# Kernel tuning notes

Hardware: AMD Instinct MI355X
Metric: run time of the kernel (lower is better)

Reference implementation:

```python
import jax, jax.numpy as jnp
import numpy as np

B, L, D = 16, 2048, 256
N_POS = (L - 24) // 16            # 126 chunk boundary positions
MAX_SEGS = L // 2 + N_POS + 2     # static upper bound on segments per utterance (=1152)


def setup_inputs() -> dict:
    key = jax.random.key(0)
    k1, k2 = jax.random.split(key, 2)
    xs_pad = jax.random.normal(k1, (B, L, D), jnp.float32)
    olens = jnp.full((B,), L, dtype=jnp.int32)
    w_lin = jax.random.normal(k2, (D, 1), jnp.float32) * 0.05
    b_lin = jnp.zeros((1,), jnp.float32)
    gamma = jnp.ones((D,), jnp.float32)
    beta = jnp.zeros((D,), jnp.float32)
    return {"xs_pad": xs_pad, "olens": olens, "w_lin": w_lin,
            "b_lin": b_lin, "gamma": gamma, "beta": beta}


def _uma_forward(xs_pad, w_lin, b_lin, gamma, beta):
    b, length, d = xs_pad.shape
    positions = 24 + 16 * jnp.arange((length - 24) // 16)  # forced chunk boundaries
    max_segs = length // 2 + positions.shape[0] + 2

    uma = jax.nn.sigmoid(xs_pad @ w_lin + b_lin)           # [B,L,1] attention weights
    w = uma[..., 0]                                        # [B,L]
    wd = jax.lax.stop_gradient(w)                          # mask construction is detached

    # strict local minima (valleys); boundary pads behave as zeros like F.pad in torch
    prev = jnp.pad(wd[:, :-1], ((0, 0), (1, 0)))
    nxt = jnp.pad(wd[:, 1:], ((0, 0), (0, 1)))
    mask = (wd < prev) & (wd < nxt)
    mask = mask.at[:, positions].set(True)                 # chunk-wise boundaries
    mask = mask.at[:, 0].set(True)

    # chunk_counts: number of segment starts within each [start_idx, end_idx) chunk
    t = jnp.arange(length)
    seg_id = jnp.searchsorted(positions, t, side='right')  # which chunk each frame is in
    chunk_counts = jax.vmap(
        lambda m: jax.ops.segment_sum(m.astype(jnp.int32), seg_id,
                                      num_segments=positions.shape[0] + 1))(mask)

    counts = mask.sum(axis=1)                              # segments per batch item (= olens out)

    # segment start indices: sorted positions of True, padded with L for empty slots
    starts = jnp.sort(jnp.where(mask, t, length), axis=1)[:, :max_segs]   # [B,M]
    # segment end indices: start-mask minus index 0, plus index L-1, then +2 clamped to L
    emask = mask.at[:, 0].set(False).at[:, -1].set(True)
    ends = jnp.minimum(jnp.sort(jnp.where(emask, t, length), axis=1)[:, :max_segs] + 2, length)
    ends = jnp.where(starts == length, length, ends)       # padded slots -> empty segment

    # segment sums over [start, end) via exclusive prefix sums (same math as tril-mask bmm)
    alpha_h = uma * xs_pad                                 # [B,L,D]
    pc_x = jnp.pad(jnp.cumsum(alpha_h, axis=1), ((0, 0), (1, 0), (0, 0)))  # [B,L+1,D]
    pc_w = jnp.pad(jnp.cumsum(w, axis=1), ((0, 0), (1, 0)))                # [B,L+1]
    bidx = jnp.arange(b)[:, None]
    num = pc_x[bidx, ends] - pc_x[bidx, starts]            # [B,M,D]
    den = pc_w[bidx, ends] - pc_w[bidx, starts]            # [B,M]
    out = num / jnp.maximum(den, 1e-6)[..., None]

    # LayerNorm (torch default eps=1e-5)
    mu = out.mean(-1, keepdims=True)
    var = ((out - mu) ** 2).mean(-1, keepdims=True)
    out = (out - mu) / jnp.sqrt(var + 1e-5) * gamma + beta
    return out, counts, chunk_counts


def reference(xs_pad, olens, w_lin, b_lin, gamma, beta):
    return _uma_forward(xs_pad, w_lin, b_lin, gamma, beta)
```

## Files before the change

kernel.cpp:

```cpp
#include <hip/hip_runtime.h>
#include <math.h>

#define BB 16
#define LL 2048
#define DD 256
#define NPOS 126
#define NSEG 127
#define MS 1152
#define POS_MAX (24 + 16 * (NPOS - 1))


__global__ __launch_bounds__(256) void k_proj(const float* __restrict__ xs,
                                              const float* __restrict__ w_lin,
                                              const float* __restrict__ b_lin,
                                              float* __restrict__ w) {
    int gtid = blockIdx.x * 256 + threadIdx.x;
    int row  = gtid >> 6;
    int lane = threadIdx.x & 63;
    const float4 x4 = *(const float4*)(xs + (size_t)row * DD + lane * 4);
    const float4 wl = *(const float4*)(w_lin + lane * 4);
    float p = x4.x * wl.x + x4.y * wl.y + x4.z * wl.z + x4.w * wl.w;
    #pragma unroll
    for (int off = 32; off > 0; off >>= 1) p += __shfl_down(p, off, 64);
    if (lane == 0) {
        float x = p + b_lin[0];
        float s = (x >= 0.f) ? 1.f / (1.f + expf(-x))
                             : expf(x) / (1.f + expf(x));
        w[row] = s;
    }
}

__global__ __launch_bounds__(256) void k_mask(const float* __restrict__ w,
                                              int* __restrict__ starts,
                                              int* __restrict__ counts_i,
                                              float* __restrict__ out_counts,
                                              float* __restrict__ out_cc) {
    int b   = blockIdx.x;
    int tid = threadIdx.x;
    __shared__ float sw[LL];
    __shared__ int   scc[NSEG];
    __shared__ int   wave_tot[4];

    for (int i = tid; i < LL; i += 256) sw[i] = w[b * LL + i];
    for (int i = tid; i < NSEG; i += 256) scc[i] = 0;
    __syncthreads();

    int base_t = tid * 8;
    bool bits[8];
    int c = 0;
    #pragma unroll
    for (int j = 0; j < 8; ++j) {
        int t = base_t + j;
        float wd = sw[t];
        float pv = (t > 0)      ? sw[t - 1] : 0.f;
        float nx = (t < LL - 1) ? sw[t + 1] : 0.f;
        bool m = (wd < pv) && (wd < nx);
        if (t == 0) m = true;
        if (t >= 24 && t <= POS_MAX && ((t - 24) & 15) == 0) m = true;
        bits[j] = m;
        c += m ? 1 : 0;
    }

    int lane = tid & 63, wv = tid >> 6;
    int inc = c;
    #pragma unroll
    for (int off = 1; off < 64; off <<= 1) {
        int v = __shfl_up(inc, off, 64);
        if (lane >= off) inc += v;
    }
    if (lane == 63) wave_tot[wv] = inc;
    __syncthreads();
    int wbase = 0;
    for (int i = 0; i < wv; ++i) wbase += wave_tot[i];
    int total = wave_tot[0] + wave_tot[1] + wave_tot[2] + wave_tot[3];
    int rank  = wbase + inc - c;

    #pragma unroll
    for (int j = 0; j < 8; ++j) {
        if (bits[j]) {
            int t = base_t + j;
            starts[b * MS + rank] = t;
            ++rank;
            int sid = (t < 24) ? 0 : min((t - 24) / 16 + 1, NSEG - 1);
            atomicAdd(&scc[sid], 1);
        }
    }
    if (tid == 0) { counts_i[b] = total; out_counts[b] = (float)total; }
    __syncthreads();
    for (int i = total + tid; i < MS; i += 256) starts[b * MS + i] = LL;
    for (int i = tid; i < NSEG; i += 256) out_cc[b * NSEG + i] = (float)scc[i];
}

__global__ __launch_bounds__(256) void k_segs(const float* __restrict__ xs,
                                              const float* __restrict__ w,
                                              const int* __restrict__ starts,
                                              const int* __restrict__ counts_i,
                                              const float* __restrict__ gamma,
                                              const float* __restrict__ beta,
                                              float* __restrict__ out) {
    int gtid = blockIdx.x * 256 + threadIdx.x;
    int seg  = gtid >> 6;
    int lane = threadIdx.x & 63;
    int b = seg / MS, k = seg - b * MS;
    int cnt = counts_i[b];
    float* orow = out + (size_t)seg * DD + lane * 4;
    if (k >= cnt) {
        *(float4*)orow = make_float4(0.f, 0.f, 0.f, 0.f);
        return;
    }
    int start = starts[b * MS + k];
    int end   = (k + 1 < cnt) ? min(starts[b * MS + k + 1] + 2, LL) : LL;

    float4 acc = make_float4(0.f, 0.f, 0.f, 0.f);
    float den = 0.f;
    const float* xrow = xs + ((size_t)(b * LL + start)) * DD + lane * 4;
    for (int t = start; t < end; ++t, xrow += DD) {
        float wt = w[b * LL + t];
        float4 x4 = *(const float4*)xrow;
        acc.x += wt * x4.x; acc.y += wt * x4.y;
        acc.z += wt * x4.z; acc.w += wt * x4.w;
        den += wt;
    }
    float inv = 1.f / fmaxf(den, 1e-6f);
    float4 v = make_float4(acc.x * inv, acc.y * inv, acc.z * inv, acc.w * inv);

    float s = v.x + v.y + v.z + v.w;
    #pragma unroll
    for (int off = 32; off > 0; off >>= 1) s += __shfl_down(s, off, 64);
    s = __shfl(s, 0, 64);
    float mu = s * (1.f / DD);
    float dx = v.x - mu, dy = v.y - mu, dz = v.z - mu, dw = v.w - mu;
    float q = dx * dx + dy * dy + dz * dz + dw * dw;
    #pragma unroll
    for (int off = 32; off > 0; off >>= 1) q += __shfl_down(q, off, 64);
    q = __shfl(q, 0, 64);
    float rstd = rsqrtf(q * (1.f / DD) + 1e-5f);

    float4 g  = *(const float4*)(gamma + lane * 4);
    float4 bt = *(const float4*)(beta + lane * 4);
    float4 o;
    o.x = dx * rstd * g.x + bt.x;
    o.y = dy * rstd * g.y + bt.y;
    o.z = dz * rstd * g.z + bt.z;
    o.w = dw * rstd * g.w + bt.w;
    *(float4*)orow = o;
}

extern "C" void kernel_launch(void* const* d_in, const int* in_sizes, int n_in,
                              void* d_out, int out_size, void* d_ws, size_t ws_size,
                              hipStream_t stream) {
    const float* xs    = (const float*)d_in[0];
    const float* w_lin = (const float*)d_in[2];
    const float* b_lin = (const float*)d_in[3];
    const float* gamma = (const float*)d_in[4];
    const float* beta  = (const float*)d_in[5];

    float* out       = (float*)d_out;
    float* out_cnt   = out + (size_t)BB * MS * DD;
    float* out_cc    = out_cnt + BB;

    float* w         = (float*)d_ws;
    int*   starts    = (int*)((char*)d_ws + (size_t)BB * LL * 4);
    int*   counts_i  = (int*)((char*)d_ws + (size_t)BB * LL * 4 + (size_t)BB * MS * 4);

    k_proj<<<(BB * LL) / 4, 256, 0, stream>>>(xs, w_lin, b_lin, w);
    k_mask<<<BB, 256, 0, stream>>>(w, starts, counts_i, out_cnt, out_cc);
    k_segs<<<(BB * MS) / 4, 256, 0, stream>>>(xs, w, starts, counts_i,
                                              gamma, beta, out);
}
```

Measured before the change: 101.2 us.

## Fuse mask/start computation into segment pooling kernel with redundant per-block scan

Merges the per-batch mask/prefix-scan kernel and the segment pooling+LayerNorm kernel into one launch. Each of 72 blocks per batch item recomputes the valley mask and start indices into shared memory, then handles 16 segment slots, reading weights from shared memory. This drops one launch, the serialized 16-block mask kernel and the global round trip for starts/counts. In exchange the scan is done redundantly per block and there are fewer, longer-running blocks.

```diff
diff --git a/kernel.cpp b/kernel.cpp
--- a/kernel.cpp
+++ b/kernel.cpp
@@ -8,6 +8,8 @@
 #define NSEG 127
 #define MS 1152
 #define POS_MAX (24 + 16 * (NPOS - 1))
+#define SB 72
+#define SLOTS 16
 
 
 __global__ __launch_bounds__(256) void k_proj(const float* __restrict__ xs,
@@ -30,19 +32,26 @@
     }
 }
 
-__global__ __launch_bounds__(256) void k_mask(const float* __restrict__ w,
-                                              int* __restrict__ starts,
-                                              int* __restrict__ counts_i,
-                                              float* __restrict__ out_counts,
-                                              float* __restrict__ out_cc) {
-    int b   = blockIdx.x;
+__global__ __launch_bounds__(256) void k_fused(const float* __restrict__ xs,
+                                               const float* __restrict__ w,
+                                               const float* __restrict__ gamma,
+                                               const float* __restrict__ beta,
+                                               float* __restrict__ out,
+                                               float* __restrict__ out_counts,
+                                               float* __restrict__ out_cc) {
+    int bx = blockIdx.x;
+    int b  = bx / SB;
+    int sb = bx - b * SB;
     int tid = threadIdx.x;
+    int lane = tid & 63, wv = tid >> 6;
+
     __shared__ float sw[LL];
+    __shared__ int   sstarts[MS];
     __shared__ int   scc[NSEG];
     __shared__ int   wave_tot[4];
 
     for (int i = tid; i < LL; i += 256) sw[i] = w[b * LL + i];
-    for (int i = tid; i < NSEG; i += 256) scc[i] = 0;
+    if (sb == 0) for (int i = tid; i < NSEG; i += 256) scc[i] = 0;
     __syncthreads();
 
     int base_t = tid * 8;
@@ -61,7 +70,6 @@
         c += m ? 1 : 0;
     }
 
-    int lane = tid & 63, wv = tid >> 6;
     int inc = c;
     #pragma unroll
     for (int off = 1; off < 64; off <<= 1) {
@@ -79,71 +87,68 @@
     for (int j = 0; j < 8; ++j) {
         if (bits[j]) {
             int t = base_t + j;
-            starts[b * MS + rank] = t;
+            sstarts[rank] = t;
             ++rank;
-            int sid = (t < 24) ? 0 : min((t - 24) / 16 + 1, NSEG - 1);
-            atomicAdd(&scc[sid], 1);
+            if (sb == 0) {
+                int sid = (t < 24) ? 0 : min((t - 24) / 16 + 1, NSEG - 1);
+                atomicAdd(&scc[sid], 1);
+            }
         }
     }
-    if (tid == 0) { counts_i[b] = total; out_counts[b] = (float)total; }
+    for (int i = total + tid; i < MS; i += 256) sstarts[i] = LL;
     __syncthreads();
-    for (int i = total + tid; i < MS; i += 256) starts[b * MS + i] = LL;
-    for (int i = tid; i < NSEG; i += 256) out_cc[b * NSEG + i] = (float)scc[i];
-}
 
-__global__ __launch_bounds__(256) void k_segs(const float* __restrict__ xs,
-                                              const float* __restrict__ w,
-                                              const int* __restrict__ starts,
-                                              const int* __restrict__ counts_i,
-                                              const float* __restrict__ gamma,
-                                              const float* __restrict__ beta,
-                                              float* __restrict__ out) {
-    int gtid = blockIdx.x * 256 + threadIdx.x;
-    int seg  = gtid >> 6;
-    int lane = threadIdx.x & 63;
-    int b = seg / MS, k = seg - b * MS;
-    int cnt = counts_i[b];
-    float* orow = out + (size_t)seg * DD + lane * 4;
-    if (k >= cnt) {
-        *(float4*)orow = make_float4(0.f, 0.f, 0.f, 0.f);
-        return;
+    if (sb == 0) {
+        if (tid == 0) out_counts[b] = (float)total;
+        for (int i = tid; i < NSEG; i += 256) out_cc[b * NSEG + i] = (float)scc[i];
     }
-    int start = starts[b * MS + k];
-    int end   = (k + 1 < cnt) ? min(starts[b * MS + k + 1] + 2, LL) : LL;
 
-    float4 acc = make_float4(0.f, 0.f, 0.f, 0.f);
-    float den = 0.f;
-    const float* xrow = xs + ((size_t)(b * LL + start)) * DD + lane * 4;
-    for (int t = start; t < end; ++t, xrow += DD) {
-        float wt = w[b * LL + t];
-        float4 x4 = *(const float4*)xrow;
-        acc.x += wt * x4.x; acc.y += wt * x4.y;
-        acc.z += wt * x4.z; acc.w += wt * x4.w;
-        den += wt;
+    const float4 g  = *(const float4*)(gamma + lane * 4);
+    const float4 bt = *(const float4*)(beta + lane * 4);
+    #pragma unroll
+    for (int j = 0; j < SLOTS / 4; ++j) {
+        int k = sb * SLOTS + j * 4 + wv;
+        float* orow = out + ((size_t)(b * MS + k)) * DD + lane * 4;
+        if (k >= total) {
+            *(float4*)orow = make_float4(0.f, 0.f, 0.f, 0.f);
+            continue;
+        }
+        int start = sstarts[k];
+        int end   = (k + 1 < total) ? min(sstarts[k + 1] + 2, LL) : LL;
+
+        float4 acc = make_float4(0.f, 0.f, 0.f, 0.f);
+        float den = 0.f;
+        const float* xrow = xs + ((size_t)(b * LL + start)) * DD + lane * 4;
+        for (int t = start; t < end; ++t, xrow += DD) {
+            float wt = sw[t];
+            float4 x4 = *(const float4*)xrow;
+            acc.x += wt * x4.x; acc.y += wt * x4.y;
+            acc.z += wt * x4.z; acc.w += wt * x4.w;
+            den += wt;
+        }
+        float invd = 1.f / fmaxf(den, 1e-6f);
+        float4 v = make_float4(acc.x * invd, acc.y * invd,
+                               acc.z * invd, acc.w * invd);
+
+        float s = v.x + v.y + v.z + v.w;
+        #pragma unroll
+        for (int off = 32; off > 0; off >>= 1) s += __shfl_down(s, off, 64);
+        s = __shfl(s, 0, 64);
+        float mu = s * (1.f / DD);
+        float dx = v.x - mu, dy = v.y - mu, dz = v.z - mu, dw = v.w - mu;
+        float q = dx * dx + dy * dy + dz * dz + dw * dw;
+        #pragma unroll
+        for (int off = 32; off > 0; off >>= 1) q += __shfl_down(q, off, 64);
+        q = __shfl(q, 0, 64);
+        float rstd = rsqrtf(q * (1.f / DD) + 1e-5f);
+
+        float4 o;
+        o.x = dx * rstd * g.x + bt.x;
+        o.y = dy * rstd * g.y + bt.y;
+        o.z = dz * rstd * g.z + bt.z;
+        o.w = dw * rstd * g.w + bt.w;
+        *(float4*)orow = o;
     }
-    float inv = 1.f / fmaxf(den, 1e-6f);
-    float4 v = make_float4(acc.x * inv, acc.y * inv, acc.z * inv, acc.w * inv);
-
-    float s = v.x + v.y + v.z + v.w;
-    #pragma unroll
-    for (int off = 32; off > 0; off >>= 1) s += __shfl_down(s, off, 64);
-    s = __shfl(s, 0, 64);
-    float mu = s * (1.f / DD);
-    float dx = v.x - mu, dy = v.y - mu, dz = v.z - mu, dw = v.w - mu;
-    float q = dx * dx + dy * dy + dz * dz + dw * dw;
-    #pragma unroll
-    for (int off = 32; off > 0; off >>= 1) q += __shfl_down(q, off, 64);
-    q = __shfl(q, 0, 64);
-    float rstd = rsqrtf(q * (1.f / DD) + 1e-5f);
-
-    float4 g  = *(const float4*)(gamma + lane * 4);
-    float4 bt = *(const float4*)(beta + lane * 4);
-    float4 o;
-    o.x = dx * rstd * g.x + bt.x;
-    o.y = dy * rstd * g.y + bt.y;
-    o.z = dz * rstd * g.z + bt.z;
-    o.w = dw * rstd * g.w + bt.w;
-    *(float4*)orow = o;
 }
 
 extern "C" void kernel_launch(void* const* d_in, const int* in_sizes, int n_in,
@@ -160,11 +165,8 @@
     float* out_cc    = out_cnt + BB;
 
     float* w         = (float*)d_ws;
-    int*   starts    = (int*)((char*)d_ws + (size_t)BB * LL * 4);
-    int*   counts_i  = (int*)((char*)d_ws + (size_t)BB * LL * 4 + (size_t)BB * MS * 4);
 
     k_proj<<<(BB * LL) / 4, 256, 0, stream>>>(xs, w_lin, b_lin, w);
-    k_mask<<<BB, 256, 0, stream>>>(w, starts, counts_i, out_cnt, out_cc);
-    k_segs<<<(BB * MS) / 4, 256, 0, stream>>>(xs, w, starts, counts_i,
-                                              gamma, beta, out);
+    k_fused<<<BB * SB, 256, 0, stream>>>(xs, w, gamma, beta,
+                                         out, out_cnt, out_cc);
 }
```

Measured after the change: 102.9 us. No clear change (+1.7%).
